# Kernel tuning notes

Hardware: AMD Instinct MI355X
Metric: run time of the kernel (lower is better)

The kernel has to match this reference:

```python
import jax, jax.numpy as jnp
import numpy as np

N_NODES = 50000
BN_EPS = 1e-5


def graph_conv(x, row, col, ew, n):
    # deg from source indices only (matches torch.bincount(row))
    deg = jnp.zeros((n,), x.dtype).at[row].add(1.0)
    dinv = jnp.where(deg > 0, deg ** -0.5, 0.0)
    norm = dinv[row] * ew * dinv[col]                     # [E]
    msg = norm[:, None] * x[row]                          # [E, F]
    return jax.ops.segment_sum(msg, col, num_segments=n)  # out[dst] += w * x[src]


def batch_norm(x, gamma, beta):
    # training-mode BN over the node (batch) dim, biased variance
    mu = jnp.mean(x, axis=0)
    var = jnp.mean((x - mu) ** 2, axis=0)
    return (x - mu) / jnp.sqrt(var + BN_EPS) * gamma + beta


def setup_inputs() -> dict:
    key = jax.random.key(0)
    ks = jax.random.split(key, 12)
    node_features = jax.random.normal(ks[0], (N_NODES, 100), dtype=jnp.float32)
    edge_index = jax.random.randint(ks[1], (2, 800000), 0, N_NODES, dtype=jnp.int64)
    edge_weights = jax.random.uniform(ks[2], (800000,), dtype=jnp.float32)
    def lin(k, fi, fo):
        lim = 1.0 / np.sqrt(fi)
        k1, k2 = jax.random.split(k)
        W = jax.random.uniform(k1, (fi, fo), minval=-lim, maxval=lim, dtype=jnp.float32)
        b = jax.random.uniform(k2, (fo,), minval=-lim, maxval=lim, dtype=jnp.float32)
        return W, b
    W0, b0 = lin(ks[3], 100, 128)
    W1, b1 = lin(ks[4], 128, 128)
    W2, b2 = lin(ks[5], 128, 64)
    return {
        "node_features": node_features, "edge_index": edge_index, "edge_weights": edge_weights,
        "W0": W0, "b0": b0, "g0": jnp.ones((128,), jnp.float32), "be0": jnp.zeros((128,), jnp.float32),
        "W1": W1, "b1": b1, "g1": jnp.ones((128,), jnp.float32), "be1": jnp.zeros((128,), jnp.float32),
        "W2": W2, "b2": b2,
    }


def reference(node_features, edge_index, edge_weights,
              W0, b0, g0, be0, W1, b1, g1, be1, W2, b2):
    n = node_features.shape[0]
    row, col = edge_index[0], edge_index[1]
    x = node_features
    # layer 0
    x = graph_conv(x, row, col, edge_weights, n)
    x = jax.nn.relu(batch_norm(x @ W0 + b0, g0, be0))
    # layer 1
    x = graph_conv(x, row, col, edge_weights, n)
    x = jax.nn.relu(batch_norm(x @ W1 + b1, g1, be1))
    # final layer (no BN/relu)
    x = graph_conv(x, row, col, edge_weights, n)
    return x @ W2 + b2
```

## Files before the change

kernel.cpp:

```cpp
#include <hip/hip_runtime.h>
#include <cstdint>

#define F0 100
#define FH 128
#define FO 64
#define PD 4
#define BN_EPS 1e-5f

typedef unsigned short ushort_t;
typedef unsigned int uint_t;
typedef __attribute__((ext_vector_type(8))) __bf16 bf16x8;
typedef __attribute__((ext_vector_type(4))) float f32x4;

static inline int ceil_div(long long a, long long b) { return (int)((a + b - 1) / b); }

__device__ __forceinline__ float bf_lo(uint_t w) { return __uint_as_float(w << 16); }
__device__ __forceinline__ float bf_hi(uint_t w) { return __uint_as_float(w & 0xffff0000u); }
__device__ __forceinline__ uint_t f2bf(float f) {
  uint_t u = __float_as_uint(f);
  return (u + 0x7fffu + ((u >> 16) & 1u)) >> 16;
}
__device__ __forceinline__ uint_t pack2(float a, float b) {
  return f2bf(a) | (f2bf(b) << 16);
}


template <int K, int F, int TM, int BK, bool BN_A, bool A_BF16, bool OUT_BF16>
__device__ __forceinline__ void gemm2_body(int bid, const void* __restrict__ A_,
                                           const float* __restrict__ W,
                                           const float* __restrict__ bias,
                                           const float* __restrict__ scA,
                                           const float* __restrict__ shA,
                                           void* __restrict__ out_, int n) {
  constexpr int NCG = F / 4;
  constexpr int NRG = 256 / NCG;
  constexpr int BR = NRG * TM;
  constexpr int F4 = F / 4;

  __shared__ float sW[BK][F];
  __shared__ float sA[BR][BK];

  const int tid = threadIdx.x;
  const int cg = tid % NCG;
  const int rg = tid / NCG;
  const int row0 = bid * BR;

  float4 acc[TM];
#pragma unroll
  for (int t = 0; t < TM; ++t) acc[t] = make_float4(0.f, 0.f, 0.f, 0.f);

  const float4* W4 = (const float4*)W;
  const float4 z4 = make_float4(0.f, 0.f, 0.f, 0.f);

  for (int k0 = 0; k0 < K; k0 += BK) {
    for (int i = tid; i < BK * F4; i += 256) {
      int kk = i / F4, f4 = i % F4;
      int gk = k0 + kk;
      ((float4*)&sW[kk][0])[f4] = (gk < K) ? W4[(size_t)gk * F4 + f4] : z4;
    }
    for (int i = tid; i < BR * (BK / 4); i += 256) {
      int r = i / (BK / 4), k4 = i % (BK / 4);
      int gr = row0 + r;
      int gk = k0 + k4 * 4;
      float4 av = z4;
      if (gr < n && gk + 3 < K) {
        if (A_BF16) {
          uint2 u = ((const uint2*)A_)[(size_t)gr * (K / 4) + (gk >> 2)];
          av.x = bf_lo(u.x); av.y = bf_hi(u.x);
          av.z = bf_lo(u.y); av.w = bf_hi(u.y);
        } else {
          av = ((const float4*)A_)[(size_t)gr * (K / 4) + (gk >> 2)];
        }
        if (BN_A) {
          float4 sc = ((const float4*)scA)[gk >> 2];
          float4 sh = ((const float4*)shA)[gk >> 2];
          av.x = fmaxf(fmaf(av.x, sc.x, sh.x), 0.f);
          av.y = fmaxf(fmaf(av.y, sc.y, sh.y), 0.f);
          av.z = fmaxf(fmaf(av.z, sc.z, sh.z), 0.f);
          av.w = fmaxf(fmaf(av.w, sc.w, sh.w), 0.f);
        }
      }
      ((float4*)&sA[r][0])[k4] = av;
    }
    __syncthreads();
#pragma unroll 4
    for (int kk = 0; kk < BK; ++kk) {
      float4 w = ((const float4*)&sW[kk][0])[cg];
#pragma unroll
      for (int t = 0; t < TM; ++t) {
        float a = sA[rg * TM + t][kk];
        acc[t].x = fmaf(a, w.x, acc[t].x);
        acc[t].y = fmaf(a, w.y, acc[t].y);
        acc[t].z = fmaf(a, w.z, acc[t].z);
        acc[t].w = fmaf(a, w.w, acc[t].w);
      }
    }
    __syncthreads();
  }

  float4 bb = bias ? ((const float4*)bias)[cg] : z4;
#pragma unroll
  for (int t = 0; t < TM; ++t) {
    int gr = row0 + rg * TM + t;
    if (gr < n) {
      float4 v = acc[t];
      v.x += bb.x; v.y += bb.y; v.z += bb.z; v.w += bb.w;
      if (OUT_BF16) {
        ((uint2*)out_)[(size_t)gr * F4 + cg] = make_uint2(pack2(v.x, v.y), pack2(v.z, v.w));
      } else {
        ((float4*)out_)[(size_t)gr * F4 + cg] = v;
      }
    }
  }
}


template <int FOUT, bool BN_A>
__global__ __launch_bounds__(256) void gemm_mfma_kernel(const ushort_t* __restrict__ A,
                                                        const float* __restrict__ W,
                                                        const float* __restrict__ bias,
                                                        const float* __restrict__ scA,
                                                        const float* __restrict__ shA,
                                                        ushort_t* __restrict__ out, int n) {
  constexpr int F4 = FOUT / 4;
  constexpr int NT = FOUT / 16;
  __shared__ ushort_t Wt[16 * FOUT * 8];

  const int tid = threadIdx.x;
  const float4* W4 = (const float4*)W;
  uint_t* w32 = (uint_t*)Wt;
  for (int idx = tid; idx < 64 * F4; idx += 256) {
    int kp = idx / F4, cq = idx % F4;
    float4 wa = W4[(size_t)(2 * kp) * F4 + cq];
    float4 wb = W4[(size_t)(2 * kp + 1) * F4 + cq];
    int kq = kp >> 2, e2 = kp & 3;
    int base = (kq * FOUT + cq * 4) * 4 + e2;
    w32[base]      = pack2(wa.x, wb.x);
    w32[base + 4]  = pack2(wa.y, wb.y);
    w32[base + 8]  = pack2(wa.z, wb.z);
    w32[base + 12] = pack2(wa.w, wb.w);
  }
  __syncthreads();

  const int l = tid & 63;
  const int wv = tid >> 6;
  const int cc = l & 15;
  const int h = l >> 4;
  const int rowa = blockIdx.x * 64 + wv * 16 + cc;
  const int ra = (rowa < n) ? rowa : (n - 1);

  f32x4 acc[NT];
#pragma unroll
  for (int t = 0; t < NT; ++t) acc[t] = (f32x4)0.f;

#pragma unroll
  for (int ks = 0; ks < 4; ++ks) {
    const int k0 = 32 * ks;
    uint4 av = *(const uint4*)(A + (size_t)ra * FH + k0 + 8 * h);
    if (BN_A) {
      const float4* sc4 = (const float4*)(scA + k0 + 8 * h);
      const float4* sh4 = (const float4*)(shA + k0 + 8 * h);
      float4 sa = sc4[0], sb = sc4[1], ha = sh4[0], hb = sh4[1];
      av.x = pack2(fmaxf(fmaf(bf_lo(av.x), sa.x, ha.x), 0.f),
                   fmaxf(fmaf(bf_hi(av.x), sa.y, ha.y), 0.f));
      av.y = pack2(fmaxf(fmaf(bf_lo(av.y), sa.z, ha.z), 0.f),
                   fmaxf(fmaf(bf_hi(av.y), sa.w, ha.w), 0.f));
      av.z = pack2(fmaxf(fmaf(bf_lo(av.z), sb.x, hb.x), 0.f),
                   fmaxf(fmaf(bf_hi(av.z), sb.y, hb.y), 0.f));
      av.w = pack2(fmaxf(fmaf(bf_lo(av.w), sb.z, hb.z), 0.f),
                   fmaxf(fmaf(bf_hi(av.w), sb.w, hb.w), 0.f));
    }
    bf16x8 afrag = __builtin_bit_cast(bf16x8, av);
    const int kq = ks * 4 + h;
#pragma unroll
    for (int ct = 0; ct < NT; ++ct) {
      int c = ct * 16 + cc;
      uint4 bv = *(const uint4*)(Wt + ((size_t)kq * FOUT + c) * 8);
      bf16x8 bfrag = __builtin_bit_cast(bf16x8, bv);
      acc[ct] = __builtin_amdgcn_mfma_f32_16x16x32_bf16(afrag, bfrag, acc[ct], 0, 0, 0);
    }
  }

  const int rbase = blockIdx.x * 64 + wv * 16 + 4 * h;
#pragma unroll
  for (int ct = 0; ct < NT; ++ct) {
    int c = ct * 16 + cc;
    float bvv = bias ? bias[c] : 0.f;
#pragma unroll
    for (int r = 0; r < 4; ++r) {
      int gr = rbase + r;
      if (gr < n) out[(size_t)gr * FOUT + c] = (ushort_t)f2bf(acc[ct][r] + bvv);
    }
  }
}


__global__ __launch_bounds__(256) void fused_gemm_hist_kernel(
    const float* __restrict__ A, const float* __restrict__ W, void* __restrict__ out, int n,
    int GB, const int* __restrict__ row, const int* __restrict__ col,
    int* __restrict__ degr_p, int* __restrict__ degc_p, int* __restrict__ posw, int E) {
  int bid = blockIdx.x;
  int r5 = bid % 5;
  int g = bid / 5;
  if (r5 == 0 && g < GB) {
    gemm2_body<F0, FH, 8, 16, false, false, true>(g, A, W, nullptr, nullptr, nullptr, out, n);
    return;
  }
  int h = (r5 == 0) ? (bid - GB) : (bid - (g + 1));
  int e = h * 256 + threadIdx.x;
  if (e >= E) return;
  atomicAdd(&degr_p[(size_t)row[e] * PD], 1);
  posw[e] = atomicAdd(&degc_p[(size_t)col[e] * PD], 1);
}


__global__ __launch_bounds__(256) void scan_fused_kernel(const int* __restrict__ degr_p,
                                                         const int* __restrict__ degc_p,
                                                         float* __restrict__ dinv,
                                                         int* __restrict__ startp,
                                                         int* __restrict__ bsums, int n,
                                                         int* __restrict__ ctr) {
  __shared__ int s[256];
  const int tid = threadIdx.x;
  int i = blockIdx.x * 256 + tid;
  int dc = 0;
  if (i < n) {
    int dr = degr_p[(size_t)i * PD];
    dc = degc_p[(size_t)i * PD];
    dinv[i] = (dr > 0) ? rsqrtf((float)dr) : 0.0f;
  }
  s[tid] = dc;
  __syncthreads();
  for (int off = 1; off < 256; off <<= 1) {
    int t = 0;
    if (tid >= off) t = s[tid - off];
    __syncthreads();
    if (tid >= off) s[tid] += t;
    __syncthreads();
  }
  if (i < n) startp[i] = s[tid] - dc;
  if (tid == 255) bsums[blockIdx.x] = s[255];
  __threadfence();
  __syncthreads();
  __shared__ int lastFlag;
  if (tid == 0) lastFlag = (atomicAdd(ctr, 1) == (int)gridDim.x - 1) ? 1 : 0;
  __syncthreads();
  if (!lastFlag) return;
  int nb = (int)gridDim.x;
  int v = (tid < nb) ? atomicAdd(&bsums[tid], 0) : 0;
  s[tid] = v;
  __syncthreads();
  for (int off = 1; off < 256; off <<= 1) {
    int t = 0;
    if (tid >= off) t = s[tid - off];
    __syncthreads();
    if (tid >= off) s[tid] += t;
    __syncthreads();
  }
  if (tid < nb) bsums[tid] = s[tid] - v;
}


__global__ __launch_bounds__(256) void csr_scatter2_kernel(const int* __restrict__ row,
                                                           const int* __restrict__ col,
                                                           const float* __restrict__ ew,
                                                           const float* __restrict__ dinv,
                                                           const int* __restrict__ startp,
                                                           const int* __restrict__ bsums,
                                                           const int* __restrict__ posw,
                                                           int2* __restrict__ ep, int E) {
  int e = blockIdx.x * blockDim.x + threadIdx.x;
  if (e >= E) return;
  int r = row[e], c = col[e];
  int pos = startp[c] + bsums[c >> 8] + posw[e];
  float coef = dinv[r] * ew[e] * dinv[c];
  ep[pos] = make_int2(r, __float_as_int(coef));
}


template <int F, bool DO_BN, bool OUT_F32>
__global__ __launch_bounds__(256) void conv_kernel(const ushort_t* __restrict__ x,
                                                   const int* __restrict__ startp,
                                                   const int* __restrict__ bsums,
                                                   const int* __restrict__ degc_p,
                                                   const int2* __restrict__ ep,
                                                   const float* __restrict__ bias,
                                                   const float* __restrict__ scale,
                                                   const float* __restrict__ shift,
                                                   void* __restrict__ out, int n) {
  constexpr int G2 = F / 8;
  constexpr int TPD = G2 / 2;
  long long tid = (long long)blockIdx.x * 256 + threadIdx.x;
  if (tid >= (long long)n * TPD) return;
  int dst = (int)(tid / TPD);
  int q = (int)(tid % TPD);
  int s0 = startp[dst] + bsums[dst >> 8];
  int d = degc_p[(size_t)dst * PD];
  const uint4* x4 = (const uint4*)x;

  float sc[16], sh[16];
  if (DO_BN) {
#pragma unroll
    for (int ch = 0; ch < 2; ++ch) {
      int g = q + ch * TPD;
#pragma unroll
      for (int j = 0; j < 8; ++j) {
        sc[ch * 8 + j] = scale[g * 8 + j];
        sh[ch * 8 + j] = shift[g * 8 + j];
      }
    }
  }

  float acc[16];
#pragma unroll
  for (int j = 0; j < 16; ++j) acc[j] = 0.f;

  for (int k = 0; k < d; ++k) {
    int2 e = ep[s0 + k];
    float c = __int_as_float(e.y);
    const uint4* xp = x4 + (size_t)e.x * G2 + q;
    uint4 v0 = xp[0];
    uint4 v1 = xp[TPD];
    uint_t vv[8] = {v0.x, v0.y, v0.z, v0.w, v1.x, v1.y, v1.z, v1.w};
#pragma unroll
    for (int hh = 0; hh < 8; ++hh) {
      float f0 = bf_lo(vv[hh]);
      float f1 = bf_hi(vv[hh]);
      if (DO_BN) {
        f0 = fmaxf(fmaf(f0, sc[2 * hh], sh[2 * hh]), 0.f);
        f1 = fmaxf(fmaf(f1, sc[2 * hh + 1], sh[2 * hh + 1]), 0.f);
      }
      acc[2 * hh] = fmaf(c, f0, acc[2 * hh]);
      acc[2 * hh + 1] = fmaf(c, f1, acc[2 * hh + 1]);
    }
  }

  if (bias) {
#pragma unroll
    for (int ch = 0; ch < 2; ++ch) {
      int g = q + ch * TPD;
#pragma unroll
      for (int j = 0; j < 8; ++j) acc[ch * 8 + j] += bias[g * 8 + j];
    }
  }

  if (OUT_F32) {
    float4* o4 = (float4*)out;
    size_t base = (size_t)dst * (F / 4);
    o4[base + 2 * q] = make_float4(acc[0], acc[1], acc[2], acc[3]);
    o4[base + 2 * q + 1] = make_float4(acc[4], acc[5], acc[6], acc[7]);
    o4[base + 2 * (q + TPD)] = make_float4(acc[8], acc[9], acc[10], acc[11]);
    o4[base + 2 * (q + TPD) + 1] = make_float4(acc[12], acc[13], acc[14], acc[15]);
  } else {
    uint4* o4 = (uint4*)out;
    size_t base = (size_t)dst * G2;
    o4[base + q] = make_uint4(pack2(acc[0], acc[1]), pack2(acc[2], acc[3]),
                              pack2(acc[4], acc[5]), pack2(acc[6], acc[7]));
    o4[base + q + TPD] = make_uint4(pack2(acc[8], acc[9]), pack2(acc[10], acc[11]),
                                    pack2(acc[12], acc[13]), pack2(acc[14], acc[15]));
  }
}


__global__ __launch_bounds__(256) void bn_stats_fast_kernel(const ushort_t* __restrict__ z,
                                                            float* __restrict__ sum,
                                                            float* __restrict__ sumsq,
                                                            const float* __restrict__ g,
                                                            const float* __restrict__ be,
                                                            float* __restrict__ scale,
                                                            float* __restrict__ shift,
                                                            int n, int* __restrict__ ctr) {
  const int tid = threadIdx.x;
  const int q = tid & 15;
  const int rg = tid >> 4;
  const uint4* z4 = (const uint4*)z;

  float s[8], s2[8];
#pragma unroll
  for (int j = 0; j < 8; ++j) { s[j] = 0.f; s2[j] = 0.f; }

  for (int r = blockIdx.x * 16 + rg; r < n; r += (int)gridDim.x * 16) {
    uint4 v = z4[(size_t)r * (FH / 8) + q];
    uint_t vv[4] = {v.x, v.y, v.z, v.w};
#pragma unroll
    for (int h = 0; h < 4; ++h) {
      float f0 = bf_lo(vv[h]);
      float f1 = bf_hi(vv[h]);
      s[2 * h] += f0;      s2[2 * h] += f0 * f0;
      s[2 * h + 1] += f1;  s2[2 * h + 1] += f1 * f1;
    }
  }

  __shared__ float red[256][8];
#pragma unroll
  for (int j = 0; j < 8; ++j) red[tid][j] = s[j];
  __syncthreads();
  for (int off = 128; off >= 16; off >>= 1) {
    if (tid < off) {
#pragma unroll
      for (int j = 0; j < 8; ++j) red[tid][j] += red[tid + off][j];
    }
    __syncthreads();
  }
  if (tid < 16) {
#pragma unroll
    for (int j = 0; j < 8; ++j) unsafeAtomicAdd(&sum[8 * tid + j], red[tid][j]);
  }
  __syncthreads();
#pragma unroll
  for (int j = 0; j < 8; ++j) red[tid][j] = s2[j];
  __syncthreads();
  for (int off = 128; off >= 16; off >>= 1) {
    if (tid < off) {
#pragma unroll
      for (int j = 0; j < 8; ++j) red[tid][j] += red[tid + off][j];
    }
    __syncthreads();
  }
  if (tid < 16) {
#pragma unroll
    for (int j = 0; j < 8; ++j) unsafeAtomicAdd(&sumsq[8 * tid + j], red[tid][j]);
  }
  __threadfence();
  __syncthreads();
  __shared__ int lastFlag;
  if (tid == 0) lastFlag = (atomicAdd(ctr, 1) == (int)gridDim.x - 1) ? 1 : 0;
  __syncthreads();
  if (lastFlag && tid < FH) {
    float S = atomicAdd(&sum[tid], 0.0f);
    float S2 = atomicAdd(&sumsq[tid], 0.0f);
    float invN = 1.0f / (float)n;
    float mean = S * invN;
    float var = fmaxf(S2 * invN - mean * mean, 0.0f);
    float sc = g[tid] / sqrtf(var + BN_EPS);
    scale[tid] = sc;
    shift[tid] = be[tid] - mean * sc;
  }
}


extern "C" void kernel_launch(void* const* d_in, const int* in_sizes, int n_in,
                              void* d_out, int out_size, void* d_ws, size_t ws_size,
                              hipStream_t stream) {
  const float* x   = (const float*)d_in[0];
  const int*   ei  = (const int*)d_in[1];
  const float* ew  = (const float*)d_in[2];
  const float* W0  = (const float*)d_in[3];
  const float* b0  = (const float*)d_in[4];
  const float* g0  = (const float*)d_in[5];
  const float* be0 = (const float*)d_in[6];
  const float* W1  = (const float*)d_in[7];
  const float* b1  = (const float*)d_in[8];
  const float* g1  = (const float*)d_in[9];
  const float* be1 = (const float*)d_in[10];
  const float* W2  = (const float*)d_in[11];
  const float* b2  = (const float*)d_in[12];

  const int n = in_sizes[0] / F0;
  const int E = in_sizes[2];
  const int* row = ei;
  const int* col = ei + E;

  ushort_t* bufA  = (ushort_t*)d_ws;
  ushort_t* bufB  = bufA + (size_t)n * FH;
  int2*   ep      = (int2*)(bufB + (size_t)n * FH);
  int*    degc_p  = (int*)(ep + E);
  int*    degr_p  = degc_p + (size_t)n * PD;
  float*  sum0    = (float*)(degr_p + (size_t)n * PD);
  float*  sumsq0  = sum0 + FH;
  float*  sum1    = sumsq0 + FH;
  float*  sumsq1  = sum1 + FH;
  int*    ctr     = (int*)(sumsq1 + FH);
  const size_t zero_bytes = (2 * (size_t)n * PD + 4 * FH + 3) * 4;
  int*    startp  = ctr + 3;
  float*  dinv    = (float*)(startp + n);
  int*    bsums   = (int*)(dinv + n);
  float*  scale0  = (float*)(bsums + 256);
  float*  shift0  = scale0 + FH;
  float*  scale1  = shift0 + FH;
  float*  shift1  = scale1 + FH;
  int*    posw    = (int*)bufB;

  const int nb = ceil_div(n, 256);
  const int GB = ceil_div(n, 64);
  const int HB = ceil_div(E, 256);
  const int MB = ceil_div(n, 64);
  const int CB_H = ceil_div((long long)n * (FH / 16), 256);
  const int CB_O = ceil_div((long long)n * (FO / 16), 256);

  (void)hipMemsetAsync(degc_p, 0, zero_bytes, stream);
  fused_gemm_hist_kernel<<<GB + HB, 256, 0, stream>>>(x, W0, bufA, n, GB, row, col,
                                                      degr_p, degc_p, posw, E);
  scan_fused_kernel<<<nb, 256, 0, stream>>>(degr_p, degc_p, dinv, startp, bsums, n, ctr + 0);
  csr_scatter2_kernel<<<HB, 256, 0, stream>>>(row, col, ew, dinv, startp, bsums, posw, ep, E);
  conv_kernel<FH, false, false><<<CB_H, 256, 0, stream>>>(
      bufA, startp, bsums, degc_p, ep, b0, nullptr, nullptr, bufB, n);
  bn_stats_fast_kernel<<<128, 256, 0, stream>>>(bufB, sum0, sumsq0, g0, be0, scale0, shift0,
                                                n, ctr + 1);
  conv_kernel<FH, true, false><<<CB_H, 256, 0, stream>>>(
      bufB, startp, bsums, degc_p, ep, nullptr, scale0, shift0, bufA, n);
  gemm_mfma_kernel<FH, false><<<MB, 256, 0, stream>>>(bufA, W1, b1, nullptr, nullptr, bufB, n);
  bn_stats_fast_kernel<<<128, 256, 0, stream>>>(bufB, sum1, sumsq1, g1, be1, scale1, shift1,
                                                n, ctr + 2);
  gemm_mfma_kernel<FO, true><<<MB, 256, 0, stream>>>(bufB, W2, nullptr, scale1, shift1, bufA, n);
  conv_kernel<FO, false, true><<<CB_O, 256, 0, stream>>>(
      bufA, startp, bsums, degc_p, ep, b2, nullptr, nullptr, (float*)d_out, n);
}
```

Before: 342.6 us.

## Privatize degree histograms per XCC to avoid cross-die atomic contention

The degree histograms are split into eight copies, one per XCC, selected by reading the hardware XCC id. Each edge atomically increments its own XCC's copy using workgroup-scope relaxed atomics, and records that copy index in the top bits of its slot offset. The scan kernel sums the copies, and a new copyoff kernel computes per-copy base offsets so the CSR scatter can place each edge. This is meant to keep histogram atomics local to each XCC's L2 instead of contending device-wide, at the cost of an extra kernel launch, eight-fold histogram memory to zero and read, and reliance on XCC-id semantics for correctness.

```diff
diff --git a/kernel.cpp b/kernel.cpp
--- a/kernel.cpp
+++ b/kernel.cpp
@@ -4,7 +4,7 @@
 #define F0 100
 #define FH 128
 #define FO 64
-#define PD 4
+#define NCPY 8
 #define BN_EPS 1e-5f
 
 typedef unsigned short ushort_t;
@@ -24,13 +24,17 @@
   return f2bf(a) | (f2bf(b) << 16);
 }
 
-
-template <int K, int F, int TM, int BK, bool BN_A, bool A_BF16, bool OUT_BF16>
+__device__ __forceinline__ int xcc_copy() {
+  int v;
+  asm volatile("s_getreg_b32 %0, hwreg(20, 0, 32)" : "=s"(v));
+  return v & (NCPY - 1);
+}
+
+
+template <int K, int F, int TM, int BK, bool A_BF16, bool OUT_BF16>
 __device__ __forceinline__ void gemm2_body(int bid, const void* __restrict__ A_,
                                            const float* __restrict__ W,
                                            const float* __restrict__ bias,
-                                           const float* __restrict__ scA,
-                                           const float* __restrict__ shA,
                                            void* __restrict__ out_, int n) {
   constexpr int NCG = F / 4;
   constexpr int NRG = 256 / NCG;
@@ -70,14 +74,6 @@
           av.z = bf_lo(u.y); av.w = bf_hi(u.y);
         } else {
           av = ((const float4*)A_)[(size_t)gr * (K / 4) + (gk >> 2)];
-        }
-        if (BN_A) {
-          float4 sc = ((const float4*)scA)[gk >> 2];
-          float4 sh = ((const float4*)shA)[gk >> 2];
-          av.x = fmaxf(fmaf(av.x, sc.x, sh.x), 0.f);
-          av.y = fmaxf(fmaf(av.y, sc.y, sh.y), 0.f);
-          av.z = fmaxf(fmaf(av.z, sc.z, sh.z), 0.f);
-          av.w = fmaxf(fmaf(av.w, sc.w, sh.w), 0.f);
         }
       }
       ((float4*)&sA[r][0])[k4] = av;
@@ -198,35 +194,47 @@
 __global__ __launch_bounds__(256) void fused_gemm_hist_kernel(
     const float* __restrict__ A, const float* __restrict__ W, void* __restrict__ out, int n,
     int GB, const int* __restrict__ row, const int* __restrict__ col,
-    int* __restrict__ degr_p, int* __restrict__ degc_p, int* __restrict__ posw, int E) {
+    int* __restrict__ degr_cp, int* __restrict__ degc_cp, int* __restrict__ posw, int E,
+    int cstride) {
   int bid = blockIdx.x;
   int r5 = bid % 5;
   int g = bid / 5;
   if (r5 == 0 && g < GB) {
-    gemm2_body<F0, FH, 8, 16, false, false, true>(g, A, W, nullptr, nullptr, nullptr, out, n);
+    gemm2_body<F0, FH, 8, 16, false, true>(g, A, W, nullptr, out, n);
     return;
   }
   int h = (r5 == 0) ? (bid - GB) : (bid - (g + 1));
   int e = h * 256 + threadIdx.x;
   if (e >= E) return;
-  atomicAdd(&degr_p[(size_t)row[e] * PD], 1);
-  posw[e] = atomicAdd(&degc_p[(size_t)col[e] * PD], 1);
-}
-
-
-__global__ __launch_bounds__(256) void scan_fused_kernel(const int* __restrict__ degr_p,
-                                                         const int* __restrict__ degc_p,
+  int j = xcc_copy();
+  int r = row[e], c = col[e];
+  __hip_atomic_fetch_add(&degr_cp[(size_t)j * cstride + r], 1, __ATOMIC_RELAXED,
+                         __HIP_MEMORY_SCOPE_WORKGROUP);
+  int pos = __hip_atomic_fetch_add(&degc_cp[(size_t)j * cstride + c], 1, __ATOMIC_RELAXED,
+                                   __HIP_MEMORY_SCOPE_WORKGROUP);
+  posw[e] = pos | (j << 28);
+}
+
+
+__global__ __launch_bounds__(256) void scan_fused_kernel(const int* __restrict__ degr_cp,
+                                                         const int* __restrict__ degc_cp,
+                                                         int* __restrict__ degc,
                                                          float* __restrict__ dinv,
                                                          int* __restrict__ startp,
                                                          int* __restrict__ bsums, int n,
-                                                         int* __restrict__ ctr) {
+                                                         int cstride, int* __restrict__ ctr) {
   __shared__ int s[256];
   const int tid = threadIdx.x;
   int i = blockIdx.x * 256 + tid;
   int dc = 0;
   if (i < n) {
-    int dr = degr_p[(size_t)i * PD];
-    dc = degc_p[(size_t)i * PD];
+    int dr = 0;
+#pragma unroll
+    for (int j = 0; j < NCPY; ++j) {
+      dr += degr_cp[(size_t)j * cstride + i];
+      dc += degc_cp[(size_t)j * cstride + i];
+    }
+    degc[i] = dc;
     dinv[i] = (dr > 0) ? rsqrtf((float)dr) : 0.0f;
   }
   s[tid] = dc;
@@ -261,18 +269,36 @@
 }
 
 
+__global__ __launch_bounds__(256) void copyoff_kernel(const int* __restrict__ startp,
+                                                      const int* __restrict__ bsums,
+                                                      const int* __restrict__ degc_cp,
+                                                      int* __restrict__ copyOff, int n,
+                                                      int cstride) {
+  int i = blockIdx.x * 256 + threadIdx.x;
+  if (i >= n) return;
+  int base = startp[i] + bsums[i >> 8];
+#pragma unroll
+  for (int j = 0; j < NCPY; ++j) {
+    copyOff[(size_t)j * cstride + i] = base;
+    base += degc_cp[(size_t)j * cstride + i];
+  }
+}
+
+
 __global__ __launch_bounds__(256) void csr_scatter2_kernel(const int* __restrict__ row,
                                                            const int* __restrict__ col,
                                                            const float* __restrict__ ew,
                                                            const float* __restrict__ dinv,
-                                                           const int* __restrict__ startp,
-                                                           const int* __restrict__ bsums,
+                                                           const int* __restrict__ copyOff,
                                                            const int* __restrict__ posw,
-                                                           int2* __restrict__ ep, int E) {
+                                                           int2* __restrict__ ep, int E,
+                                                           int cstride) {
   int e = blockIdx.x * blockDim.x + threadIdx.x;
   if (e >= E) return;
   int r = row[e], c = col[e];
-  int pos = startp[c] + bsums[c >> 8] + posw[e];
+  int pw = posw[e];
+  int j = pw >> 28;
+  int pos = copyOff[(size_t)j * cstride + c] + (pw & 0x0FFFFFFF);
   float coef = dinv[r] * ew[e] * dinv[c];
   ep[pos] = make_int2(r, __float_as_int(coef));
 }
@@ -282,7 +308,7 @@
 __global__ __launch_bounds__(256) void conv_kernel(const ushort_t* __restrict__ x,
                                                    const int* __restrict__ startp,
                                                    const int* __restrict__ bsums,
-                                                   const int* __restrict__ degc_p,
+                                                   const int* __restrict__ degc,
                                                    const int2* __restrict__ ep,
                                                    const float* __restrict__ bias,
                                                    const float* __restrict__ scale,
@@ -295,7 +321,7 @@
   int dst = (int)(tid / TPD);
   int q = (int)(tid % TPD);
   int s0 = startp[dst] + bsums[dst >> 8];
-  int d = degc_p[(size_t)dst * PD];
+  int d = degc[dst];
   const uint4* x4 = (const uint4*)x;
 
   float sc[16], sh[16];
@@ -460,22 +486,25 @@
   const int E = in_sizes[2];
   const int* row = ei;
   const int* col = ei + E;
+  const int cstride = (n + 63) & ~63;
 
   ushort_t* bufA  = (ushort_t*)d_ws;
   ushort_t* bufB  = bufA + (size_t)n * FH;
   int2*   ep      = (int2*)(bufB + (size_t)n * FH);
-  int*    degc_p  = (int*)(ep + E);
-  int*    degr_p  = degc_p + (size_t)n * PD;
-  float*  sum0    = (float*)(degr_p + (size_t)n * PD);
+  int*    degc_cp = (int*)(ep + E);
+  int*    degr_cp = degc_cp + (size_t)NCPY * cstride;
+  float*  sum0    = (float*)(degr_cp + (size_t)NCPY * cstride);
   float*  sumsq0  = sum0 + FH;
   float*  sum1    = sumsq0 + FH;
   float*  sumsq1  = sum1 + FH;
   int*    ctr     = (int*)(sumsq1 + FH);
-  const size_t zero_bytes = (2 * (size_t)n * PD + 4 * FH + 3) * 4;
+  const size_t zero_bytes = (2 * (size_t)NCPY * cstride + 4 * FH + 3) * 4;
   int*    startp  = ctr + 3;
-  float*  dinv    = (float*)(startp + n);
+  int*    degc    = startp + n;
+  float*  dinv    = (float*)(degc + n);
   int*    bsums   = (int*)(dinv + n);
-  float*  scale0  = (float*)(bsums + 256);
+  int*    copyOff = bsums + 256;
+  float*  scale0  = (float*)(copyOff + (size_t)NCPY * cstride);
   float*  shift0  = scale0 + FH;
   float*  scale1  = shift0 + FH;
   float*  shift1  = scale1 + FH;
@@ -488,21 +517,23 @@
   const int CB_H = ceil_div((long long)n * (FH / 16), 256);
   const int CB_O = ceil_div((long long)n * (FO / 16), 256);
 
-  (void)hipMemsetAsync(degc_p, 0, zero_bytes, stream);
+  (void)hipMemsetAsync(degc_cp, 0, zero_bytes, stream);
   fused_gemm_hist_kernel<<<GB + HB, 256, 0, stream>>>(x, W0, bufA, n, GB, row, col,
-                                                      degr_p, degc_p, posw, E);
-  scan_fused_kernel<<<nb, 256, 0, stream>>>(degr_p, degc_p, dinv, startp, bsums, n, ctr + 0);
-  csr_scatter2_kernel<<<HB, 256, 0, stream>>>(row, col, ew, dinv, startp, bsums, posw, ep, E);
+                                                      degr_cp, degc_cp, posw, E, cstride);
+  scan_fused_kernel<<<nb, 256, 0, stream>>>(degr_cp, degc_cp, degc, dinv, startp, bsums, n,
+                                            cstride, ctr + 0);
+  copyoff_kernel<<<nb, 256, 0, stream>>>(startp, bsums, degc_cp, copyOff, n, cstride);
+  csr_scatter2_kernel<<<HB, 256, 0, stream>>>(row, col, ew, dinv, copyOff, posw, ep, E, cstride);
   conv_kernel<FH, false, false><<<CB_H, 256, 0, stream>>>(
-      bufA, startp, bsums, degc_p, ep, b0, nullptr, nullptr, bufB, n);
+      bufA, startp, bsums, degc, ep, b0, nullptr, nullptr, bufB, n);
   bn_stats_fast_kernel<<<128, 256, 0, stream>>>(bufB, sum0, sumsq0, g0, be0, scale0, shift0,
                                                 n, ctr + 1);
   conv_kernel<FH, true, false><<<CB_H, 256, 0, stream>>>(
-      bufB, startp, bsums, degc_p, ep, nullptr, scale0, shift0, bufA, n);
+      bufB, startp, bsums, degc, ep, nullptr, scale0, shift0, bufA, n);
   gemm_mfma_kernel<FH, false><<<MB, 256, 0, stream>>>(bufA, W1, b1, nullptr, nullptr, bufB, n);
   bn_stats_fast_kernel<<<128, 256, 0, stream>>>(bufB, sum1, sumsq1, g1, be1, scale1, shift1,
                                                 n, ctr + 2);
   gemm_mfma_kernel<FO, true><<<MB, 256, 0, stream>>>(bufB, W2, nullptr, scale1, shift1, bufA, n);
   conv_kernel<FO, false, true><<<CB_O, 256, 0, stream>>>(
-      bufA, startp, bsums, degc_p, ep, b2, nullptr, nullptr, (float*)d_out, n);
-}
+      bufA, startp, bsums, degc, ep, b2, nullptr, nullptr, (float*)d_out, n);
+}
```

Result: no change. 344.6 us (+0.6%).

## Slice graph conv by feature blocks so the gathered working set fits in cache

Applied to the files above, without the earlier changes.

Replaces the conv kernel with a feature-sliced version. Blocks are grouped by 32-feature slice (64 bytes per source row in bf16), and each slice sweeps all destination nodes. The gathered source data per pass is therefore a quarter (or half) of the full feature table and is more likely to stay in L2/MALL. Two threads per node each handle 16 contiguous features. Edge records are read with nontemporal loads, and the unused BN_A path in the gemm helper is removed. The cost is that each edge list is traversed once per slice, multiplying index and coefficient reads.

```diff
diff --git a/kernel.cpp b/kernel.cpp
--- a/kernel.cpp
+++ b/kernel.cpp
@@ -25,12 +25,10 @@
 }
 
 
-template <int K, int F, int TM, int BK, bool BN_A, bool A_BF16, bool OUT_BF16>
+template <int K, int F, int TM, int BK, bool A_BF16, bool OUT_BF16>
 __device__ __forceinline__ void gemm2_body(int bid, const void* __restrict__ A_,
                                            const float* __restrict__ W,
                                            const float* __restrict__ bias,
-                                           const float* __restrict__ scA,
-                                           const float* __restrict__ shA,
                                            void* __restrict__ out_, int n) {
   constexpr int NCG = F / 4;
   constexpr int NRG = 256 / NCG;
@@ -70,14 +68,6 @@
           av.z = bf_lo(u.y); av.w = bf_hi(u.y);
         } else {
           av = ((const float4*)A_)[(size_t)gr * (K / 4) + (gk >> 2)];
-        }
-        if (BN_A) {
-          float4 sc = ((const float4*)scA)[gk >> 2];
-          float4 sh = ((const float4*)shA)[gk >> 2];
-          av.x = fmaxf(fmaf(av.x, sc.x, sh.x), 0.f);
-          av.y = fmaxf(fmaf(av.y, sc.y, sh.y), 0.f);
-          av.z = fmaxf(fmaf(av.z, sc.z, sh.z), 0.f);
-          av.w = fmaxf(fmaf(av.w, sc.w, sh.w), 0.f);
         }
       }
       ((float4*)&sA[r][0])[k4] = av;
@@ -203,7 +193,7 @@
   int r5 = bid % 5;
   int g = bid / 5;
   if (r5 == 0 && g < GB) {
-    gemm2_body<F0, FH, 8, 16, false, false, true>(g, A, W, nullptr, nullptr, nullptr, out, n);
+    gemm2_body<F0, FH, 8, 16, false, true>(g, A, W, nullptr, out, n);
     return;
   }
   int h = (r5 == 0) ? (bid - GB) : (bid - (g + 1));
@@ -278,86 +268,86 @@
 }
 
 
-template <int F, bool DO_BN, bool OUT_F32>
-__global__ __launch_bounds__(256) void conv_kernel(const ushort_t* __restrict__ x,
-                                                   const int* __restrict__ startp,
-                                                   const int* __restrict__ bsums,
-                                                   const int* __restrict__ degc_p,
-                                                   const int2* __restrict__ ep,
-                                                   const float* __restrict__ bias,
-                                                   const float* __restrict__ scale,
-                                                   const float* __restrict__ shift,
-                                                   void* __restrict__ out, int n) {
+template <int F, int NSLICE, bool DO_BN, bool OUT_F32>
+__global__ __launch_bounds__(256) void conv_slice_kernel(const ushort_t* __restrict__ x,
+                                                         const int* __restrict__ startp,
+                                                         const int* __restrict__ bsums,
+                                                         const int* __restrict__ degc_p,
+                                                         const int2* __restrict__ ep,
+                                                         const float* __restrict__ bias,
+                                                         const float* __restrict__ scale,
+                                                         const float* __restrict__ shift,
+                                                         void* __restrict__ out, int n,
+                                                         int BPS) {
   constexpr int G2 = F / 8;
-  constexpr int TPD = G2 / 2;
-  long long tid = (long long)blockIdx.x * 256 + threadIdx.x;
-  if (tid >= (long long)n * TPD) return;
-  int dst = (int)(tid / TPD);
-  int q = (int)(tid % TPD);
-  int s0 = startp[dst] + bsums[dst >> 8];
-  int d = degc_p[(size_t)dst * PD];
+  constexpr int SQ = G2 / NSLICE;
+  static_assert(SQ == 4, "slice must be 4 uint4 chunks (32 features)");
+  const int s = blockIdx.x / BPS;
+  const int rem = blockIdx.x % BPS;
+  const int local = rem * 256 + threadIdx.x;
+  if (local >= 2 * n) return;
+  const int dst = local >> 1;
+  const int h2 = local & 1;
+  const int cq = s * SQ + h2 * 2;
+  const int f0 = cq * 8;
+
+  const int s0 = startp[dst] + bsums[dst >> 8];
+  const int d = degc_p[(size_t)dst * PD];
   const uint4* x4 = (const uint4*)x;
 
   float sc[16], sh[16];
   if (DO_BN) {
 #pragma unroll
-    for (int ch = 0; ch < 2; ++ch) {
-      int g = q + ch * TPD;
-#pragma unroll
-      for (int j = 0; j < 8; ++j) {
-        sc[ch * 8 + j] = scale[g * 8 + j];
-        sh[ch * 8 + j] = shift[g * 8 + j];
+    for (int j = 0; j < 16; ++j) {
+      sc[j] = scale[f0 + j];
+      sh[j] = shift[f0 + j];
+    }
+  }
+
+  float acc[16];
+#pragma unroll
+  for (int j = 0; j < 16; ++j) acc[j] = 0.f;
+
+  for (int k = 0; k < d; ++k) {
+    long long ev = __builtin_nontemporal_load((const long long*)(ep + s0 + k));
+    int src = (int)(uint_t)(ev & 0xffffffffll);
+    float c = __int_as_float((int)(ev >> 32));
+    const uint4* xp = x4 + (size_t)src * G2 + cq;
+    uint4 v0 = xp[0];
+    uint4 v1 = xp[1];
+    uint_t vv[8] = {v0.x, v0.y, v0.z, v0.w, v1.x, v1.y, v1.z, v1.w};
+#pragma unroll
+    for (int hh = 0; hh < 8; ++hh) {
+      float g0 = bf_lo(vv[hh]);
+      float g1 = bf_hi(vv[hh]);
+      if (DO_BN) {
+        g0 = fmaxf(fmaf(g0, sc[2 * hh], sh[2 * hh]), 0.f);
+        g1 = fmaxf(fmaf(g1, sc[2 * hh + 1], sh[2 * hh + 1]), 0.f);
       }
-    }
-  }
-
-  float acc[16];
-#pragma unroll
-  for (int j = 0; j < 16; ++j) acc[j] = 0.f;
-
-  for (int k = 0; k < d; ++k) {
-    int2 e = ep[s0 + k];
-    float c = __int_as_float(e.y);
-    const uint4* xp = x4 + (size_t)e.x * G2 + q;
-    uint4 v0 = xp[0];
-    uint4 v1 = xp[TPD];
-    uint_t vv[8] = {v0.x, v0.y, v0.z, v0.w, v1.x, v1.y, v1.z, v1.w};
-#pragma unroll
-    for (int hh = 0; hh < 8; ++hh) {
-      float f0 = bf_lo(vv[hh]);
-      float f1 = bf_hi(vv[hh]);
-      if (DO_BN) {
-        f0 = fmaxf(fmaf(f0, sc[2 * hh], sh[2 * hh]), 0.f);
-        f1 = fmaxf(fmaf(f1, sc[2 * hh + 1], sh[2 * hh + 1]), 0.f);
-      }
-      acc[2 * hh] = fmaf(c, f0, acc[2 * hh]);
-      acc[2 * hh + 1] = fmaf(c, f1, acc[2 * hh + 1]);
+      acc[2 * hh] = fmaf(c, g0, acc[2 * hh]);
+      acc[2 * hh + 1] = fmaf(c, g1, acc[2 * hh + 1]);
     }
   }
 
   if (bias) {
 #pragma unroll
-    for (int ch = 0; ch < 2; ++ch) {
-      int g = q + ch * TPD;
-#pragma unroll
-      for (int j = 0; j < 8; ++j) acc[ch * 8 + j] += bias[g * 8 + j];
-    }
+    for (int j = 0; j < 16; ++j) acc[j] += bias[f0 + j];
   }
 
   if (OUT_F32) {
     float4* o4 = (float4*)out;
-    size_t base = (size_t)dst * (F / 4);
-    o4[base + 2 * q] = make_float4(acc[0], acc[1], acc[2], acc[3]);
-    o4[base + 2 * q + 1] = make_float4(acc[4], acc[5], acc[6], acc[7]);
-    o4[base + 2 * (q + TPD)] = make_float4(acc[8], acc[9], acc[10], acc[11]);
-    o4[base + 2 * (q + TPD) + 1] = make_float4(acc[12], acc[13], acc[14], acc[15]);
+    size_t base = (size_t)dst * (F / 4) + cq * 2;
+    o4[base + 0] = make_float4(acc[0], acc[1], acc[2], acc[3]);
+    o4[base + 1] = make_float4(acc[4], acc[5], acc[6], acc[7]);
+    o4[base + 2] = make_float4(acc[8], acc[9], acc[10], acc[11]);
+    o4[base + 3] = make_float4(acc[12], acc[13], acc[14], acc[15]);
   } else {
     uint4* o4 = (uint4*)out;
-    size_t base = (size_t)dst * G2;
-    o4[base + q] = make_uint4(pack2(acc[0], acc[1]), pack2(acc[2], acc[3]),
+    size_t base = (size_t)dst * G2 + cq;
+    o4[base + 0] = make_uint4(pack2(acc[0], acc[1]), pack2(acc[2], acc[3]),
                               pack2(acc[4], acc[5]), pack2(acc[6], acc[7]));
-    o4[base + q + TPD] = make_uint4(pack2(acc[8], acc[9]), pack2(acc[10], acc[11]),
-                                    pack2(acc[12], acc[13]), pack2(acc[14], acc[15]));
+    o4[base + 1] = make_uint4(pack2(acc[8], acc[9]), pack2(acc[10], acc[11]),
+                              pack2(acc[12], acc[13]), pack2(acc[14], acc[15]));
   }
 }
 
@@ -485,24 +475,23 @@
   const int GB = ceil_div(n, 64);
   const int HB = ceil_div(E, 256);
   const int MB = ceil_div(n, 64);
-  const int CB_H = ceil_div((long long)n * (FH / 16), 256);
-  const int CB_O = ceil_div((long long)n * (FO / 16), 256);
+  const int BPS = ceil_div(2 * (long long)n, 256);
 
   (void)hipMemsetAsync(degc_p, 0, zero_bytes, stream);
   fused_gemm_hist_kernel<<<GB + HB, 256, 0, stream>>>(x, W0, bufA, n, GB, row, col,
                                                       degr_p, degc_p, posw, E);
   scan_fused_kernel<<<nb, 256, 0, stream>>>(degr_p, degc_p, dinv, startp, bsums, n, ctr + 0);
   csr_scatter2_kernel<<<HB, 256, 0, stream>>>(row, col, ew, dinv, startp, bsums, posw, ep, E);
-  conv_kernel<FH, false, false><<<CB_H, 256, 0, stream>>>(
-      bufA, startp, bsums, degc_p, ep, b0, nullptr, nullptr, bufB, n);
+  conv_slice_kernel<FH, 4, false, false><<<4 * BPS, 256, 0, stream>>>(
+      bufA, startp, bsums, degc_p, ep, b0, nullptr, nullptr, bufB, n, BPS);
   bn_stats_fast_kernel<<<128, 256, 0, stream>>>(bufB, sum0, sumsq0, g0, be0, scale0, shift0,
                                                 n, ctr + 1);
-  conv_kernel<FH, true, false><<<CB_H, 256, 0, stream>>>(
-      bufB, startp, bsums, degc_p, ep, nullptr, scale0, shift0, bufA, n);
+  conv_slice_kernel<FH, 4, true, false><<<4 * BPS, 256, 0, stream>>>(
+      bufB, startp, bsums, degc_p, ep, nullptr, scale0, shift0, bufA, n, BPS);
   gemm_mfma_kernel<FH, false><<<MB, 256, 0, stream>>>(bufA, W1, b1, nullptr, nullptr, bufB, n);
   bn_stats_fast_kernel<<<128, 256, 0, stream>>>(bufB, sum1, sumsq1, g1, be1, scale1, shift1,
                                                 n, ctr + 2);
   gemm_mfma_kernel<FO, true><<<MB, 256, 0, stream>>>(bufB, W2, nullptr, scale1, shift1, bufA, n);
-  conv_kernel<FO, false, true><<<CB_O, 256, 0, stream>>>(
-      bufA, startp, bsums, degc_p, ep, b2, nullptr, nullptr, (float*)d_out, n);
-}
+  conv_slice_kernel<FO, 2, false, true><<<2 * BPS, 256, 0, stream>>>(
+      bufA, startp, bsums, degc_p, ep, b2, nullptr, nullptr, (float*)d_out, n, BPS);
+}
```

Measured after the change: 522.8 us. +52.6%, slower.
